# Kernel tuning notes

Measured on AMD Instinct MI355X. Metric: run time of the kernel, lower is better.

Reference implementation:

```python
import jax, jax.numpy as jnp
import numpy as np

L, E, S, V, B, T = 6, 768, 1024, 32000, 2, 1024
FF = 4 * E
EPS = 1e-5

def _layernorm(v, w, b):
    m = jnp.mean(v, axis=-1, keepdims=True)
    var = jnp.mean((v - m) ** 2, axis=-1, keepdims=True)
    return (v - m) * jax.lax.rsqrt(var + EPS) * w + b

def setup_inputs() -> dict:
    key = jax.random.key(0)
    ks = jax.random.split(key, 12)
    s = 0.02
    n = lambda k, shp: (jax.random.normal(k, shp, jnp.float32) * s)
    return {
        "x": jax.random.randint(ks[0], (B, T), 0, V),
        "tok_emb": n(ks[1], (V, E)),
        "pos_emb": jax.random.normal(ks[2], (S, E), jnp.float32),  # nn.Parameter(randn)
        "Wq": n(ks[3], (L, E, E)), "bq": jnp.zeros((L, E), jnp.float32),
        "Wk": n(ks[4], (L, E, E)), "bk": jnp.zeros((L, E), jnp.float32),
        "Wv": n(ks[5], (L, E, E)), "bv": jnp.zeros((L, E), jnp.float32),
        "ln1w": jnp.ones((L, E), jnp.float32), "ln1b": jnp.zeros((L, E), jnp.float32),
        "W1": n(ks[6], (L, E, FF)), "b1": jnp.zeros((L, FF), jnp.float32),
        "W2": n(ks[7], (L, FF, E)), "b2": jnp.zeros((L, E), jnp.float32),
        "ln2w": jnp.ones((L, E), jnp.float32), "ln2b": jnp.zeros((L, E), jnp.float32),
        "Wo": n(ks[8], (E, V)), "bo": jnp.zeros((V,), jnp.float32),
    }

def reference(x, tok_emb, pos_emb, Wq, bq, Wk, bk, Wv, bv, ln1w, ln1b,
              W1, b1, W2, b2, ln2w, ln2b, Wo, bo):
    t = x.shape[1]
    h = tok_emb[x] + pos_emb[:t]  # [B,T,E]
    scale = jnp.sqrt(jnp.float32(E))
    tril = jnp.tril(jnp.ones((t, t), bool))

    def layer(h, p):
        wq, bq_, wk, bk_, wv, bv_, l1w, l1b, w1, b1_, w2, b2_, l2w, l2b = p
        Q = h @ wq + bq_
        K = h @ wk + bk_
        Vv = h @ wv + bv_
        scores = jnp.einsum('btd,bsd->bts', Q, K) / scale
        # original adds a mask of 1.0 on allowed positions, -inf elsewhere
        masked = jnp.where(tril, scores + 1.0, -jnp.inf)
        A = jax.nn.softmax(masked, axis=-1)
        att = jnp.einsum('bts,bsd->btd', A, Vv)
        h1 = _layernorm(h + att, l1w, l1b)
        ffn = jax.nn.relu(h1 @ w1 + b1_) @ w2 + b2_
        h2 = _layernorm(ffn + h1, l2w, l2b)
        return h2, None

    params = (Wq, bq, Wk, bk, Wv, bv, ln1w, ln1b, W1, b1, W2, b2, ln2w, ln2b)
    h, _ = jax.lax.scan(layer, h, params)
    return h @ Wo + bo  # [B,T,V]
```

## Files before the change

### kernel.cpp

```cpp
#include <hip/hip_runtime.h>
#include <stdint.h>

typedef __bf16 v8bf __attribute__((ext_vector_type(8)));
typedef float  v4f  __attribute__((ext_vector_type(4)));

__device__ __forceinline__ float bf2f(uint16_t h) {
    union { uint32_t u; float f; } x; x.u = ((uint32_t)h) << 16; return x.f;
}
__device__ __forceinline__ uint16_t f2bf(float f) {
    union { float f; uint32_t u; } x; x.f = f;
    uint32_t r = x.u + 0x7fffu + ((x.u >> 16) & 1u);
    return (uint16_t)(r >> 16);
}

__device__ __forceinline__ void gload16(const uint16_t* g, uint16_t* l) {
    __builtin_amdgcn_global_load_lds((const __attribute__((address_space(1))) void*)g,
                                     (__attribute__((address_space(3))) void*)l, 16, 0, 0);
}

__global__ void k_embed(const int* __restrict__ x, const float* __restrict__ tok,
                        const float* __restrict__ pos, float* __restrict__ hf,
                        uint16_t* __restrict__ hb)
{
    int i = blockIdx.x;
    int t = i & 1023;
    int tk = x[i];
    const float* te = tok + (long)tk * 768;
    const float* pe = pos + (long)t * 768;
    for (int j = threadIdx.x; j < 768; j += 256) {
        float v = te[j] + pe[j];
        hf[(long)i * 768 + j] = v;
        hb[(long)i * 768 + j] = f2bf(v);
    }
}

template<typename SrcT>
__global__ void k_transpose(const SrcT* __restrict__ src, uint16_t* __restrict__ dst,
                            int ldS, int ldD, long sBatch, long dBatch)
{
    __shared__ float tile[32][33];
    src += (long)blockIdx.z * sBatch;
    dst += (long)blockIdx.z * dBatch;
    int c0 = blockIdx.x * 32, r0 = blockIdx.y * 32;
    int tx = threadIdx.x, ty = threadIdx.y;
    #pragma unroll
    for (int i = 0; i < 4; ++i) {
        int r = r0 + ty + i * 8;
        SrcT s = src[(long)r * ldS + c0 + tx];
        float v;
        if constexpr (sizeof(SrcT) == 4) v = (float)s; else v = bf2f((uint16_t)s);
        tile[ty + i * 8][tx] = v;
    }
    __syncthreads();
    #pragma unroll
    for (int i = 0; i < 4; ++i) {
        int c = c0 + ty + i * 8;
        dst[(long)c * ldD + r0 + tx] = f2bf(tile[tx][ty + i * 8]);
    }
}

__global__ void k_concat3(const float* __restrict__ a, const float* __restrict__ b,
                          const float* __restrict__ c, float* __restrict__ out)
{
    int l = blockIdx.y;
    const float* s = (blockIdx.x == 0) ? a : ((blockIdx.x == 1) ? b : c);
    s += (long)l * 768;
    for (int j = threadIdx.x; j < 768; j += 256)
        out[(long)l * 2304 + blockIdx.x * 768 + j] = s[j];
}

template<typename OutT, bool BIAS, bool RELU, bool RES>
__global__ __launch_bounds__(256, 3)
void k_gemmp(const uint16_t* __restrict__ A, const uint16_t* __restrict__ BT,
             OutT* __restrict__ C, const float* __restrict__ bias,
             const float* __restrict__ res,
             int K, int lda, int ldb, int ldc,
             long bsA, long bsB, long bsC, float scale, int causal)
{
    const int nwg = gridDim.x * gridDim.y;
    int lin = blockIdx.y * gridDim.x + blockIdx.x;
    {
        int q = nwg >> 3, r = nwg & 7, x = lin & 7, i = lin >> 3;
        lin = (x < r ? x * (q + 1) : r * (q + 1) + (x - r) * q) + i;
    }
    const int mt = lin % gridDim.y;
    const int nt = lin / gridDim.y;

    if (causal == 1 && nt * 64 >= (mt + 1) * 128) return;
    const int Keff = (causal == 2) ? ((mt + 1) * 128 < K ? (mt + 1) * 128 : K) : K;
    const int KT = Keff >> 6;

    __shared__ uint16_t lds[2][192 * 64];
    const int tid  = threadIdx.x;
    const int lane = tid & 63;
    const int bz   = blockIdx.z;
    const uint16_t* Ab = A + (long)bz * bsA + (long)mt * 128 * lda;
    const uint16_t* Bb = BT + (long)bz * bsB + (long)nt * 64 * ldb;

    const int wm = (tid >> 6) >> 1, wn = (tid >> 6) & 1;
    const int fr = lane & 15, fq = lane >> 4;

    const int srow = tid >> 3;
    const int sl   = tid & 7;

    v4f acc[4][2];
    #pragma unroll
    for (int m = 0; m < 4; ++m)
        #pragma unroll
        for (int n = 0; n < 2; ++n) acc[m][n] = (v4f){0.f, 0.f, 0.f, 0.f};

    auto stage = [&](int t, int buf) {
        const int ko = t * 64;
        #pragma unroll
        for (int p = 0; p < 6; ++p) {
            int row = p * 32 + srow;
            int ss  = (sl ^ (row & 7)) * 8;
            const uint16_t* g = (p < 4) ? (Ab + (long)row * lda + ko + ss)
                                        : (Bb + (long)(row - 128) * ldb + ko + ss);
            gload16(g, &lds[buf][p * 2048 + tid * 8]);
        }
    };

    stage(0, 0);

    for (int kti = 0; kti < KT; ++kti) {
        asm volatile("s_waitcnt vmcnt(0)" ::: "memory");
        __builtin_amdgcn_s_barrier();
        if (kti + 1 < KT) stage(kti + 1, (kti + 1) & 1);

        const uint16_t* l = &lds[kti & 1][0];
        #pragma unroll
        for (int kk = 0; kk < 2; ++kk) {
            const int sIdx = kk * 4 + fq;
            v8bf ag[4], bg[2];
            #pragma unroll
            for (int m = 0; m < 4; ++m) {
                int r = wm * 64 + m * 16 + fr;
                ag[m] = *(const v8bf*)&l[r * 64 + ((sIdx ^ (r & 7)) << 3)];
            }
            #pragma unroll
            for (int n = 0; n < 2; ++n) {
                int r = 128 + wn * 32 + n * 16 + fr;
                bg[n] = *(const v8bf*)&l[r * 64 + ((sIdx ^ (r & 7)) << 3)];
            }
            __builtin_amdgcn_s_setprio(1);
            #pragma unroll
            for (int m = 0; m < 4; ++m)
                #pragma unroll
                for (int n = 0; n < 2; ++n)
                    acc[m][n] = __builtin_amdgcn_mfma_f32_16x16x32_bf16(ag[m], bg[n], acc[m][n], 0, 0, 0);
            __builtin_amdgcn_s_setprio(0);
        }
    }

    OutT* Cb = C + (long)bz * bsC + (long)mt * 128 * ldc + nt * 64;
    const float* Rb = RES ? (res + (long)bz * bsC + (long)mt * 128 * ldc + nt * 64) : nullptr;
    #pragma unroll
    for (int n = 0; n < 2; ++n) {
        int col = wn * 32 + n * 16 + fr;
        float bv = BIAS ? bias[nt * 64 + col] : 0.f;
        #pragma unroll
        for (int m = 0; m < 4; ++m) {
            #pragma unroll
            for (int r = 0; r < 4; ++r) {
                int row = wm * 64 + m * 16 + fq * 4 + r;
                float v = acc[m][n][r] * scale + bv;
                if (RES) v += Rb[(long)row * ldc + col];
                if (RELU) v = fmaxf(v, 0.f);
                if constexpr (sizeof(OutT) == 4) Cb[(long)row * ldc + col] = v;
                else                             Cb[(long)row * ldc + col] = f2bf(v);
            }
        }
    }
}

__global__ __launch_bounds__(512, 2)
void k_glogits(const uint16_t* __restrict__ A, const uint16_t* __restrict__ BT,
               float* __restrict__ C, const float* __restrict__ bias,
               int K, int lda, int ldb, int ldc, float scale)
{
    __shared__ uint16_t lds[2][512 * 64];

    const int nwg = gridDim.x * gridDim.y;
    int lin = blockIdx.y * gridDim.x + blockIdx.x;
    {
        int q = nwg >> 3, r = nwg & 7, x = lin & 7, i = lin >> 3;
        lin = (x < r ? x * (q + 1) : r * (q + 1) + (x - r) * q) + i;
    }
    const int mt = lin % gridDim.y;
    const int nt = lin / gridDim.y;

    const int tid  = threadIdx.x;
    const int lane = tid & 63;
    const int wid  = tid >> 6;
    const int wm = wid >> 2, wn = wid & 3;
    const int fr = lane & 15, fq = lane >> 4;

    const uint16_t* Ab = A  + (long)mt * 256 * lda;
    const uint16_t* Bb = BT + (long)nt * 256 * ldb;

    const int srow = tid >> 3;
    const int sl   = tid & 7;
    const int KT   = K >> 6;

    v4f acc[8][4];
    #pragma unroll
    for (int m = 0; m < 8; ++m)
        #pragma unroll
        for (int n = 0; n < 4; ++n) acc[m][n] = (v4f){0.f, 0.f, 0.f, 0.f};

    auto stage = [&](int t, int buf) {
        const int ko = t * 64;
        #pragma unroll
        for (int p = 0; p < 8; ++p) {
            int row = p * 64 + srow;
            int ss  = (sl ^ (row & 7)) * 8;
            const uint16_t* g = (p < 4) ? (Ab + (long)row * lda + ko + ss)
                                        : (Bb + (long)(row - 256) * ldb + ko + ss);
            gload16(g, &lds[buf][p * 4096 + tid * 8]);
        }
    };

    stage(0, 0);

    for (int kti = 0; kti < KT; ++kti) {
        asm volatile("s_waitcnt vmcnt(0)" ::: "memory");
        __builtin_amdgcn_s_barrier();
        if (kti + 1 < KT) stage(kti + 1, (kti + 1) & 1);

        const uint16_t* l = &lds[kti & 1][0];
        #pragma unroll
        for (int kk = 0; kk < 2; ++kk) {
            const int sIdx = kk * 4 + fq;
            v8bf ag[8], bg[4];
            #pragma unroll
            for (int m = 0; m < 8; ++m) {
                int r = wm * 128 + m * 16 + fr;
                ag[m] = *(const v8bf*)&l[r * 64 + ((sIdx ^ (r & 7)) << 3)];
            }
            #pragma unroll
            for (int n = 0; n < 4; ++n) {
                int r = 256 + wn * 64 + n * 16 + fr;
                bg[n] = *(const v8bf*)&l[r * 64 + ((sIdx ^ (r & 7)) << 3)];
            }
            __builtin_amdgcn_s_setprio(1);
            #pragma unroll
            for (int m = 0; m < 8; ++m)
                #pragma unroll
                for (int n = 0; n < 4; ++n)
                    acc[m][n] = __builtin_amdgcn_mfma_f32_16x16x32_bf16(ag[m], bg[n], acc[m][n], 0, 0, 0);
            __builtin_amdgcn_s_setprio(0);
        }
    }

    float* Cb = C + (long)(mt * 256 + wm * 128) * ldc + nt * 256 + wn * 64;
    #pragma unroll
    for (int n = 0; n < 4; ++n) {
        int col = n * 16 + fr;
        float bv = bias[nt * 256 + wn * 64 + col];
        #pragma unroll
        for (int m = 0; m < 8; ++m) {
            #pragma unroll
            for (int r = 0; r < 4; ++r) {
                int row = m * 16 + fq * 4 + r;
                __builtin_nontemporal_store(acc[m][n][r] * scale + bv, &Cb[(long)row * ldc + col]);
            }
        }
    }
}

__global__ void k_softmax(const float* __restrict__ S, uint16_t* __restrict__ P)
{
    int t = blockIdx.x, b = blockIdx.y;
    const float* row = S + ((long)b * 1024 + t) * 1024;
    uint16_t* pr = P + ((long)b * 1024 + t) * 1024;
    int limit = (t & ~127) + 128;
    int s0 = threadIdx.x * 4;
    float vals[4] = {0.f, 0.f, 0.f, 0.f};
    if (s0 < limit) {
        float4 vv = *(const float4*)(row + s0);
        vals[0] = vv.x; vals[1] = vv.y; vals[2] = vv.z; vals[3] = vv.w;
    }
    float mx = -1e30f;
    #pragma unroll
    for (int j = 0; j < 4; ++j) if (s0 + j <= t) mx = fmaxf(mx, vals[j]);
    #pragma unroll
    for (int o = 32; o; o >>= 1) mx = fmaxf(mx, __shfl_xor(mx, o));
    __shared__ float red[8];
    int wave = threadIdx.x >> 6, lane = threadIdx.x & 63;
    if (lane == 0) red[wave] = mx;
    __syncthreads();
    mx = fmaxf(fmaxf(red[0], red[1]), fmaxf(red[2], red[3]));
    float e[4]; float sum = 0.f;
    #pragma unroll
    for (int j = 0; j < 4; ++j) { e[j] = (s0 + j <= t) ? __expf(vals[j] - mx) : 0.f; sum += e[j]; }
    #pragma unroll
    for (int o = 32; o; o >>= 1) sum += __shfl_xor(sum, o);
    if (lane == 0) red[4 + wave] = sum;
    __syncthreads();
    sum = red[4] + red[5] + red[6] + red[7];
    float inv = 1.f / sum;
    if (s0 < limit) {
        #pragma unroll
        for (int j = 0; j < 4; ++j) pr[s0 + j] = f2bf(e[j] * inv);
    }
}

__global__ void k_ln(const float* __restrict__ a,
                     const float* __restrict__ w, const float* __restrict__ bias,
                     float* __restrict__ outf, uint16_t* __restrict__ outb)
{
    int row = blockIdx.x;
    const float* ar = a + (long)row * 768;
    float v[3]; float s1 = 0.f, s2 = 0.f;
    #pragma unroll
    for (int i = 0; i < 3; ++i) {
        int e = threadIdx.x + i * 256;
        v[i] = ar[e];
        s1 += v[i]; s2 += v[i] * v[i];
    }
    #pragma unroll
    for (int o = 32; o; o >>= 1) { s1 += __shfl_xor(s1, o); s2 += __shfl_xor(s2, o); }
    __shared__ float red[8];
    int wave = threadIdx.x >> 6, lane = threadIdx.x & 63;
    if (lane == 0) { red[wave] = s1; red[4 + wave] = s2; }
    __syncthreads();
    s1 = red[0] + red[1] + red[2] + red[3];
    s2 = red[4] + red[5] + red[6] + red[7];
    float mean = s1 * (1.f / 768.f);
    float var  = s2 * (1.f / 768.f) - mean * mean;
    float rstd = rsqrtf(var + 1e-5f);
    #pragma unroll
    for (int i = 0; i < 3; ++i) {
        int e = threadIdx.x + i * 256;
        float o = (v[i] - mean) * rstd * w[e] + bias[e];
        outf[(long)row * 768 + e] = o;
        outb[(long)row * 768 + e] = f2bf(o);
    }
}

__global__ void k_ln_ffn2(const float* __restrict__ p, long pstride,
                          const float* __restrict__ b2, const float* __restrict__ h1,
                          const float* __restrict__ w, const float* __restrict__ bias,
                          float* __restrict__ outf, uint16_t* __restrict__ outb)
{
    int row = blockIdx.x;
    long base = (long)row * 768;
    float v[3]; float s1 = 0.f, s2 = 0.f;
    #pragma unroll
    for (int i = 0; i < 3; ++i) {
        int e = threadIdx.x + i * 256;
        float acc = b2[e] + h1[base + e];
        #pragma unroll
        for (int s = 0; s < 4; ++s) acc += p[base + e + s * pstride];
        v[i] = acc;
        s1 += acc; s2 += acc * acc;
    }
    #pragma unroll
    for (int o = 32; o; o >>= 1) { s1 += __shfl_xor(s1, o); s2 += __shfl_xor(s2, o); }
    __shared__ float red[8];
    int wave = threadIdx.x >> 6, lane = threadIdx.x & 63;
    if (lane == 0) { red[wave] = s1; red[4 + wave] = s2; }
    __syncthreads();
    s1 = red[0] + red[1] + red[2] + red[3];
    s2 = red[4] + red[5] + red[6] + red[7];
    float mean = s1 * (1.f / 768.f);
    float var  = s2 * (1.f / 768.f) - mean * mean;
    float rstd = rsqrtf(var + 1e-5f);
    #pragma unroll
    for (int i = 0; i < 3; ++i) {
        int e = threadIdx.x + i * 256;
        float o = (v[i] - mean) * rstd * w[e] + bias[e];
        outf[base + e] = o;
        outb[base + e] = f2bf(o);
    }
}

extern "C" void kernel_launch(void* const* d_in, const int* in_sizes, int n_in,
                              void* d_out, int out_size, void* d_ws, size_t ws_size,
                              hipStream_t stream)
{
    const int*   x       = (const int*)d_in[0];
    const float* tok_emb = (const float*)d_in[1];
    const float* pos_emb = (const float*)d_in[2];
    const float* Wq  = (const float*)d_in[3];
    const float* bq  = (const float*)d_in[4];
    const float* Wk  = (const float*)d_in[5];
    const float* bk  = (const float*)d_in[6];
    const float* Wv  = (const float*)d_in[7];
    const float* bv  = (const float*)d_in[8];
    const float* ln1w = (const float*)d_in[9];
    const float* ln1b = (const float*)d_in[10];
    const float* W1  = (const float*)d_in[11];
    const float* b1  = (const float*)d_in[12];
    const float* W2  = (const float*)d_in[13];
    const float* b2  = (const float*)d_in[14];
    const float* ln2w = (const float*)d_in[15];
    const float* ln2b = (const float*)d_in[16];
    const float* Wo  = (const float*)d_in[17];
    const float* bo  = (const float*)d_in[18];
    float* out = (float*)d_out;
    (void)in_sizes; (void)n_in; (void)out_size;

    char* ws = (char*)d_ws;
    size_t off = 0;
    auto alloc = [&](size_t bytes) -> char* {
        char* p = ws + off;
        off = (off + bytes + 255) & ~(size_t)255;
        return p;
    };
    uint16_t* WoT   = (uint16_t*)alloc(32000L * 768 * 2);
    float*    hf    = (float*)alloc(2048L * 768 * 4);
    uint16_t* hb    = (uint16_t*)alloc(2048L * 768 * 2);
    uint16_t* qkv   = (uint16_t*)alloc(2048L * 2304 * 2);
    uint16_t* vT    = (uint16_t*)alloc(2L * 768 * 1024 * 2);
    float*    sc    = (float*)alloc(2L * 1024 * 1024 * 4);
    uint16_t* pr    = (uint16_t*)alloc(2L * 1024 * 1024 * 2);
    float*    hsum  = (float*)alloc(2048L * 768 * 4);
    float*    h1f   = (float*)alloc(2048L * 768 * 4);
    uint16_t* h1b   = (uint16_t*)alloc(2048L * 768 * 2);
    uint16_t* f1    = (uint16_t*)alloc(2048L * 3072 * 2);
    float*    f2p   = (float*)alloc(4L * 2048 * 768 * 4);
    float*    bqkvA = (float*)alloc(6L * 2304 * 4);
    const long PSTR = 2048L * 768;

    size_t mark = off;
    uint16_t* WqkvTA = (uint16_t*)alloc(6L * 2304 * 768 * 2);
    uint16_t* W1TA   = (uint16_t*)alloc(6L * 3072 * 768 * 2);
    uint16_t* W2TA   = (uint16_t*)alloc(6L * 768 * 3072 * 2);
    bool hoist = (off <= ws_size);
    uint16_t *WqkvT = nullptr, *W1T = nullptr, *W2T = nullptr;
    if (!hoist) {
        off = mark;
        WqkvT = (uint16_t*)alloc(2304L * 768 * 2);
        W1T   = (uint16_t*)alloc(3072L * 768 * 2);
        W2T   = (uint16_t*)alloc(768L * 3072 * 2);
    }

    dim3 tb(32, 8);
    const float iscale = 0.036084391824351615f;
    const long EE = 768L * 768;

    k_transpose<float><<<dim3(1000, 24, 1), tb, 0, stream>>>(Wo, WoT, 32000, 768, 0, 0);
    k_embed<<<2048, 256, 0, stream>>>(x, tok_emb, pos_emb, hf, hb);
    k_concat3<<<dim3(3, 6), 256, 0, stream>>>(bq, bk, bv, bqkvA);

    if (hoist) {
        k_transpose<float><<<dim3(24, 24, 6), tb, 0, stream>>>(Wq, WqkvTA,             768, 768, EE, 2304L*768);
        k_transpose<float><<<dim3(24, 24, 6), tb, 0, stream>>>(Wk, WqkvTA + 768L*768,  768, 768, EE, 2304L*768);
        k_transpose<float><<<dim3(24, 24, 6), tb, 0, stream>>>(Wv, WqkvTA + 1536L*768, 768, 768, EE, 2304L*768);
        k_transpose<float><<<dim3(96, 24, 6), tb, 0, stream>>>(W1, W1TA, 3072, 768, 768L*3072, 3072L*768);
        k_transpose<float><<<dim3(24, 96, 6), tb, 0, stream>>>(W2, W2TA, 768, 3072, 3072L*768, 768L*3072);
    }

    for (int l = 0; l < 6; ++l) {
        uint16_t* WqkvL = hoist ? (WqkvTA + l * 2304L * 768) : WqkvT;
        uint16_t* W1L   = hoist ? (W1TA   + l * 3072L * 768) : W1T;
        uint16_t* W2L   = hoist ? (W2TA   + l * 768L * 3072) : W2T;
        if (!hoist) {
            k_transpose<float><<<dim3(24, 24, 1), tb, 0, stream>>>(Wq + l * EE, WqkvT,             768, 768, 0, 0);
            k_transpose<float><<<dim3(24, 24, 1), tb, 0, stream>>>(Wk + l * EE, WqkvT + 768L*768,  768, 768, 0, 0);
            k_transpose<float><<<dim3(24, 24, 1), tb, 0, stream>>>(Wv + l * EE, WqkvT + 1536L*768, 768, 768, 0, 0);
            k_transpose<float><<<dim3(96, 24, 1), tb, 0, stream>>>(W1 + l * 768L * 3072, W1T, 3072, 768, 0, 0);
            k_transpose<float><<<dim3(24, 96, 1), tb, 0, stream>>>(W2 + l * 3072L * 768, W2T, 768, 3072, 0, 0);
        }

        k_gemmp<uint16_t, true, false, false><<<dim3(36, 16, 1), 256, 0, stream>>>(
            hb, WqkvL, qkv, bqkvA + l * 2304, nullptr, 768, 768, 768, 2304, 0, 0, 0, 1.f, 0);
        k_gemmp<float, false, false, false><<<dim3(16, 8, 2), 256, 0, stream>>>(
            qkv, qkv + 768, sc, nullptr, nullptr, 768, 2304, 2304, 1024,
            1024L * 2304, 1024L * 2304, 1024L * 1024, iscale, 1);
        k_softmax<<<dim3(1024, 2), 256, 0, stream>>>(sc, pr);
        k_transpose<uint16_t><<<dim3(24, 32, 2), tb, 0, stream>>>(
            qkv + 1536, vT, 2304, 1024, 1024L * 2304, 768L * 1024);
        k_gemmp<float, false, false, true><<<dim3(12, 8, 2), 256, 0, stream>>>(
            pr, vT, hsum, nullptr, hf, 1024, 1024, 1024, 768,
            1024L * 1024, 768L * 1024, 1024L * 768, 1.f, 2);
        k_ln<<<2048, 256, 0, stream>>>(hsum, ln1w + l * 768, ln1b + l * 768, h1f, h1b);
        k_gemmp<uint16_t, true, true, false><<<dim3(48, 16, 1), 256, 0, stream>>>(
            h1b, W1L, f1, b1 + l * 3072, nullptr, 768, 768, 768, 3072, 0, 0, 0, 1.f, 0);
        k_gemmp<float, false, false, false><<<dim3(12, 16, 4), 256, 0, stream>>>(
            f1, W2L, f2p, nullptr, nullptr, 768, 3072, 3072, 768,
            768, 768, PSTR, 1.f, 0);
        k_ln_ffn2<<<2048, 256, 0, stream>>>(f2p, PSTR, b2 + l * 768, h1f,
                                            ln2w + l * 768, ln2b + l * 768, hf, hb);
    }

    k_glogits<<<dim3(125, 8, 1), 512, 0, stream>>>(
        hb, WoT, out, bo, 768, 768, 768, 32000, 1.f);
}
```

Measured before the change: 822.8 us.

## Restructure GEMM main loop into 8-phase half-tile staged pipeline

```diff
diff --git a/kernel.cpp b/kernel.cpp
--- a/kernel.cpp
+++ b/kernel.cpp
@@ -199,9 +199,8 @@
     const uint16_t* Ab = A  + (long)mt * 256 * lda;
     const uint16_t* Bb = BT + (long)nt * 256 * ldb;
 
-    const int srow = tid >> 3;
-    const int sl   = tid & 7;
-    const int KT   = K >> 6;
+    const int KS  = K >> 6;
+    const int NIT = KS >> 1;
 
     v4f acc[8][4];
     #pragma unroll
@@ -209,48 +208,91 @@
         #pragma unroll
         for (int n = 0; n < 4; ++n) acc[m][n] = (v4f){0.f, 0.f, 0.f, 0.f};
 
-    auto stage = [&](int t, int buf) {
-        const int ko = t * 64;
-        #pragma unroll
-        for (int p = 0; p < 8; ++p) {
-            int row = p * 64 + srow;
-            int ss  = (sl ^ (row & 7)) * 8;
-            const uint16_t* g = (p < 4) ? (Ab + (long)row * lda + ko + ss)
-                                        : (Bb + (long)(row - 256) * ldb + ko + ss);
-            gload16(g, &lds[buf][p * 4096 + tid * 8]);
+    auto stageH = [&](int op, int half, int s) {
+        if (s >= KS) return;
+        uint16_t* base = &lds[s & 1][op * 16384 + half * 8192];
+        const uint16_t* G = op ? Bb : Ab;
+        const int ld = op ? ldb : lda;
+        #pragma unroll
+        for (int u = 0; u < 2; ++u) {
+            int rowg = half * 128 + (tid >> 3) + u * 64;
+            int ss = ((tid & 7) ^ (rowg & 7)) << 3;
+            gload16(G + (long)rowg * ld + s * 64 + ss, base + (tid + u * 512) * 8);
         }
     };
 
-    stage(0, 0);
-
-    for (int kti = 0; kti < KT; ++kti) {
-        asm volatile("s_waitcnt vmcnt(0)" ::: "memory");
-        __builtin_amdgcn_s_barrier();
-        if (kti + 1 < KT) stage(kti + 1, (kti + 1) & 1);
-
-        const uint16_t* l = &lds[kti & 1][0];
-        #pragma unroll
-        for (int kk = 0; kk < 2; ++kk) {
-            const int sIdx = kk * 4 + fq;
-            v8bf ag[8], bg[4];
-            #pragma unroll
-            for (int m = 0; m < 8; ++m) {
-                int r = wm * 128 + m * 16 + fr;
-                ag[m] = *(const v8bf*)&l[r * 64 + ((sIdx ^ (r & 7)) << 3)];
+    v8bf ag[4][2], bg0[2][2], bg1[2][2];
+
+    auto readAg = [&](int buf, int mh) {
+        #pragma unroll
+        for (int m = 0; m < 4; ++m)
+            #pragma unroll
+            for (int kk = 0; kk < 2; ++kk) {
+                int r = wm * 128 + mh * 64 + m * 16 + fr;
+                ag[m][kk] = *(const v8bf*)&lds[buf][r * 64 + ((((kk << 2) | fq) ^ (r & 7)) << 3)];
             }
-            #pragma unroll
-            for (int n = 0; n < 4; ++n) {
-                int r = 256 + wn * 64 + n * 16 + fr;
-                bg[n] = *(const v8bf*)&l[r * 64 + ((sIdx ^ (r & 7)) << 3)];
+    };
+    auto readBg = [&](int buf, int nh, v8bf (&bg)[2][2]) {
+        #pragma unroll
+        for (int n = 0; n < 2; ++n)
+            #pragma unroll
+            for (int kk = 0; kk < 2; ++kk) {
+                int r = wn * 64 + nh * 32 + n * 16 + fr;
+                bg[n][kk] = *(const v8bf*)&lds[buf][16384 + r * 64 + ((((kk << 2) | fq) ^ (r & 7)) << 3)];
             }
-            __builtin_amdgcn_s_setprio(1);
-            #pragma unroll
-            for (int m = 0; m < 8; ++m)
+    };
+    auto mmaq = [&](int mh, int nh, v8bf (&bg)[2][2]) {
+        __builtin_amdgcn_s_setprio(1);
+        #pragma unroll
+        for (int m = 0; m < 4; ++m)
+            #pragma unroll
+            for (int n = 0; n < 2; ++n)
                 #pragma unroll
-                for (int n = 0; n < 4; ++n)
-                    acc[m][n] = __builtin_amdgcn_mfma_f32_16x16x32_bf16(ag[m], bg[n], acc[m][n], 0, 0, 0);
-            __builtin_amdgcn_s_setprio(0);
-        }
+                for (int kk = 0; kk < 2; ++kk)
+                    acc[mh * 4 + m][nh * 2 + n] =
+                        __builtin_amdgcn_mfma_f32_16x16x32_bf16(ag[m][kk], bg[n][kk],
+                                                                acc[mh * 4 + m][nh * 2 + n], 0, 0, 0);
+        __builtin_amdgcn_s_setprio(0);
+    };
+
+    stageH(0, 0, 0); stageH(0, 1, 0); stageH(1, 0, 0); stageH(1, 1, 0);
+    stageH(0, 0, 1);
+
+    for (int i = 0; i < NIT; ++i) {
+        const int s1 = 2 * i + 1;
+        asm volatile("s_waitcnt vmcnt(2)" ::: "memory");
+        __builtin_amdgcn_s_barrier();
+        readAg(0, 0); readBg(0, 0, bg0);
+        stageH(0, 1, s1);
+        mmaq(0, 0, bg0);
+        __builtin_amdgcn_s_barrier();
+        readBg(0, 1, bg1);
+        stageH(1, 0, s1);
+        mmaq(0, 1, bg1);
+        __builtin_amdgcn_s_barrier();
+        readAg(0, 1);
+        stageH(1, 1, s1);
+        mmaq(1, 0, bg0);
+        __builtin_amdgcn_s_barrier();
+        stageH(0, 0, s1 + 1);
+        mmaq(1, 1, bg1);
+        if (i + 1 < NIT) asm volatile("s_waitcnt vmcnt(2)" ::: "memory");
+        else             asm volatile("s_waitcnt vmcnt(0)" ::: "memory");
+        __builtin_amdgcn_s_barrier();
+        readAg(1, 0); readBg(1, 0, bg0);
+        stageH(0, 1, s1 + 1);
+        mmaq(0, 0, bg0);
+        __builtin_amdgcn_s_barrier();
+        readBg(1, 1, bg1);
+        stageH(1, 0, s1 + 1);
+        mmaq(0, 1, bg1);
+        __builtin_amdgcn_s_barrier();
+        readAg(1, 1);
+        stageH(1, 1, s1 + 1);
+        mmaq(1, 0, bg0);
+        __builtin_amdgcn_s_barrier();
+        stageH(0, 0, s1 + 2);
+        mmaq(1, 1, bg1);
     }
 
     float* Cb = C + (long)(mt * 256 + wm * 128) * ldc + nt * 256 + wn * 64;
```

Measured after the change: 821.3 us. Within noise of the previous version (-0.2%).
